# Optimization experiments

Measured on AMD Instinct MI355X. Metric: run time of the kernel, lower is better.

The kernel has to match this reference:

```python
import jax, jax.numpy as jnp
import numpy as np

B, S, T = 64, 256, 32
VS, VT = 4000, 32000
E = H = 512
L = 2
PAD_IDX = 1
BOS_IDX = 2


def setup_inputs() -> dict:
    key = jax.random.key(0)
    ks = jax.random.split(key, 16)
    u = lambda k, sh: jax.random.uniform(k, sh, jnp.float32, -0.08, 0.08)
    inp = {
        'X': jax.random.randint(ks[0], (B, S), 0, VS),
        'y': jax.random.randint(ks[1], (B, T), 0, VT),
        'emb_src': u(ks[2], (VS, E)).at[PAD_IDX].set(0.0),
        'emb_tgt': u(ks[3], (VT, E)).at[PAD_IDX].set(0.0),
        'enc_Wih': u(ks[4], (L, 4 * H, E)),
        'enc_Whh': u(ks[5], (L, 4 * H, H)),
        'enc_bih': u(ks[6], (L, 4 * H)),
        'enc_bhh': u(ks[7], (L, 4 * H)),
        'dec_Wih': u(ks[8], (L, 4 * H, E)),
        'dec_Whh': u(ks[9], (L, 4 * H, H)),
        'dec_bih': u(ks[10], (L, 4 * H)),
        'dec_bhh': u(ks[11], (L, 4 * H)),
        'fcW': u(ks[12], (VT, H)),
        'fcb': u(ks[13], (VT,)),
    }
    return inp


def _cell(x, h, c, Wih, Whh, bih, bhh):
    # PyTorch LSTM cell, gate order i,f,g,o. x:[B,E], h,c:[B,H]
    gates = x @ Wih.T + h @ Whh.T + bih + bhh  # [B,4H]
    i, f, g, o = jnp.split(gates, 4, axis=-1)
    c = jax.nn.sigmoid(f) * c + jax.nn.sigmoid(i) * jnp.tanh(g)
    h = jax.nn.sigmoid(o) * jnp.tanh(c)
    return h, c


def _stack_step(x, hs, cs, Wih, Whh, bih, bhh):
    # run num_layers stacked cells for one timestep; hs,cs: [L,B,H]
    new_h, new_c = [], []
    inp = x
    for l in range(Wih.shape[0]):
        h, c = _cell(inp, hs[l], cs[l], Wih[l], Whh[l], bih[l], bhh[l])
        new_h.append(h)
        new_c.append(c)
        inp = h
    return jnp.stack(new_h), jnp.stack(new_c), inp


def _forward(X, y, emb_src, emb_tgt, enc_Wih, enc_Whh, enc_bih, enc_bhh,
             dec_Wih, dec_Whh, dec_bih, dec_bhh, fcW, fcb):
    b = X.shape[0]
    # ----- encoder: LSTM over full (un-padded) source sequence -----
    xs = emb_src[X].transpose(1, 0, 2)  # [S,B,E] time-major
    h0 = jnp.zeros((L, b, H), xs.dtype)
    c0 = jnp.zeros((L, b, H), xs.dtype)

    def enc_step(carry, x):
        hs, cs = carry
        hs, cs, _ = _stack_step(x, hs, cs, enc_Wih, enc_Whh, enc_bih, enc_bhh)
        return (hs, cs), None

    (hs, cs), _ = jax.lax.scan(enc_step, (h0, c0), xs)

    bos = jnp.full((b, 1), BOS_IDX, y.dtype)
    dec_in = jnp.concatenate([bos, y[:, :-1]], axis=1)  # [B,T]
    toks = dec_in.transpose(1, 0)  # [T,B]

    def dec_step(carry, tok):
        hs, cs = carry
        x = emb_tgt[tok]  # [B,E]
        hs, cs, top = _stack_step(x, hs, cs, dec_Wih, dec_Whh, dec_bih, dec_bhh)
        return (hs, cs), top

    (_, _), tops = jax.lax.scan(dec_step, (hs, cs), toks)  # tops: [T,B,H]
    # model returns only the last time step's log-softmax prediction
    logits = tops[-1] @ fcW.T + fcb  # [B,VT]
    return jax.nn.log_softmax(logits, axis=-1)


def reference(X, y, emb_src, emb_tgt, enc_Wih, enc_Whh, enc_bih, enc_bhh,
              dec_Wih, dec_Whh, dec_bih, dec_bhh, fcW, fcb):
    return _forward(X, y, emb_src, emb_tgt, enc_Wih, enc_Whh, enc_bih, enc_bhh,
                    dec_Wih, dec_Whh, dec_bih, dec_bhh, fcW, fcb)
```

## Files before the change

kernel.cpp:

```cpp
#include <hip/hip_runtime.h>

#define NB 256
#define NT 256

typedef __attribute__((ext_vector_type(8))) short short8;
typedef __attribute__((ext_vector_type(4))) float f32x4;

constexpr int Bz = 64, Sz = 256, Tz = 32, Ez = 512, Hz = 512, G4 = 2048, VT = 32000;

__device__ __forceinline__ unsigned short f2b(float f) {
    unsigned u; __builtin_memcpy(&u, &f, 4);
    u = (u + 0x7fffu + ((u >> 16) & 1u)) >> 16;
    return (unsigned short)u;
}
__device__ __forceinline__ float sgm(float x) { return 1.0f / (1.0f + __expf(-x)); }
__device__ __forceinline__ float tnh(float x) { return 1.0f - 2.0f / (1.0f + __expf(2.0f * x)); }

__global__ __launch_bounds__(NT) void init_kernel(
    unsigned* __restrict__ hbuf_u32, float* __restrict__ row_sums,
    unsigned* __restrict__ bars)
{
    const int idx = blockIdx.x * NT + threadIdx.x;
#pragma unroll
    for (int i = 0; i < 4; ++i) hbuf_u32[idx * 4 + i] = 0u;
    if (blockIdx.x == 0) {
        bars[threadIdx.x] = 0u;
        if (threadIdx.x < 64) row_sums[threadIdx.x] = 0.0f;
    }
}

__global__ __launch_bounds__(NT, 2) void scan_kernel(
    const int* __restrict__ X, const int* __restrict__ Y,
    const float* __restrict__ emb_src, const float* __restrict__ emb_tgt,
    const float* __restrict__ eWih, const float* __restrict__ eWhh,
    const float* __restrict__ ebih, const float* __restrict__ ebhh,
    const float* __restrict__ dWih, const float* __restrict__ dWhh,
    const float* __restrict__ dbih, const float* __restrict__ dbhh,
    unsigned short* __restrict__ hbuf,
    unsigned* __restrict__ bars)
{
    __shared__ __align__(16) unsigned char smem[38144];
    unsigned short* xh_lds = (unsigned short*)smem;
    float* gates_lds = (float*)(smem + 33024);
    float* c_lds     = (float*)(smem + 33024 + 4096);

    const int tid  = threadIdx.x;
    const int bid  = blockIdx.x;
    const int lay  = bid >> 7;
    const int bt   = (bid >> 5) & 3;
    const int ht   = bid & 31;
    const int wave = tid >> 6;
    const int lane = tid & 63;
    const int nl   = lane & 15;
    const int quad = lane >> 4;
    const int srow = tid >> 4;
    const int ssub = tid & 15;
    const int bglob = bt * 16 + srow;

    unsigned* bar_arrive = bars + bt * 64;
    unsigned* bar_flag   = bars + bt * 64 + 32;
    unsigned gen = 0;

    auto barrier = [&]() {
        ++gen;
        __syncthreads();
        if (tid == 0) {
            unsigned old = __hip_atomic_fetch_add(bar_arrive, 1u,
                               __ATOMIC_RELAXED, __HIP_MEMORY_SCOPE_AGENT);
            if (old == gen * 64u - 1u) {
                __hip_atomic_store(bar_flag, gen,
                                   __ATOMIC_RELAXED, __HIP_MEMORY_SCOPE_AGENT);
            } else {
                while (__hip_atomic_load(bar_flag,
                           __ATOMIC_RELAXED, __HIP_MEMORY_SCOPE_AGENT) < gen)
                    __builtin_amdgcn_s_sleep(1);
            }
        }
        __syncthreads();
    };

    c_lds[tid] = 0.0f;
    __syncthreads();

    short8 wfrag[32];
    float bias_r = 0.0f;
    const int r = wave * 512 + ht * 16 + nl;

    auto load_w = [&](const float* Wih, const float* Whh,
                      const float* bih, const float* bhh) {
        const float* wi = Wih + (size_t)(lay * G4 + r) * 512;
        const float* wh = Whh + (size_t)(lay * G4 + r) * 512;
#pragma unroll
        for (int kc = 0; kc < 32; ++kc) {
            const int k0 = kc * 32 + quad * 8;
            const float* s = (k0 < 512) ? (wi + k0) : (wh + (k0 - 512));
            short8 v;
#pragma unroll
            for (int j = 0; j < 8; ++j) v[j] = (short)f2b(s[j]);
            wfrag[kc] = v;
        }
        bias_r = bih[lay * G4 + r] + bhh[lay * G4 + r];
    };

    auto step = [&](const float* xrow_f, const unsigned short* xrow_b,
                    const unsigned short* hrow, unsigned short* hout) {
        {
            unsigned short* d = xh_lds + srow * 1032;
            if (xrow_f) {
                short8* dx = (short8*)(d + ssub * 32);
                const float4* xs = (const float4*)xrow_f;
#pragma unroll
                for (int i = 0; i < 4; ++i) {
                    float4 lo = xs[ssub * 8 + 2 * i];
                    float4 hi = xs[ssub * 8 + 2 * i + 1];
                    short8 v;
                    v[0] = (short)f2b(lo.x); v[1] = (short)f2b(lo.y);
                    v[2] = (short)f2b(lo.z); v[3] = (short)f2b(lo.w);
                    v[4] = (short)f2b(hi.x); v[5] = (short)f2b(hi.y);
                    v[6] = (short)f2b(hi.z); v[7] = (short)f2b(hi.w);
                    dx[i] = v;
                }
            } else {
                const unsigned long long* xs = (const unsigned long long*)xrow_b;
                unsigned long long* dx = (unsigned long long*)(d + ssub * 32);
#pragma unroll
                for (int i = 0; i < 8; ++i)
                    dx[i] = __hip_atomic_load(xs + ssub * 8 + i,
                                __ATOMIC_RELAXED, __HIP_MEMORY_SCOPE_AGENT);
            }
            const unsigned long long* hs = (const unsigned long long*)hrow;
            unsigned long long* dh = (unsigned long long*)(d + 512 + ssub * 32);
#pragma unroll
            for (int i = 0; i < 8; ++i)
                dh[i] = __hip_atomic_load(hs + ssub * 8 + i,
                            __ATOMIC_RELAXED, __HIP_MEMORY_SCOPE_AGENT);
        }
        __syncthreads();
        f32x4 acc = {0.f, 0.f, 0.f, 0.f};
        const unsigned short* ar = xh_lds + nl * 1032 + quad * 8;
#pragma unroll
        for (int kc = 0; kc < 32; ++kc) {
            short8 a = *(const short8*)(ar + kc * 32);
            acc = __builtin_amdgcn_mfma_f32_16x16x32_bf16(a, wfrag[kc], acc, 0, 0, 0);
        }
#pragma unroll
        for (int i = 0; i < 4; ++i) {
            float v = acc[i] + bias_r;
            v = (wave == 2) ? tnh(v) : sgm(v);
            gates_lds[wave * 256 + (quad * 4 + i) * 16 + nl] = v;
        }
        __syncthreads();
        if (tid < 128) {
            const int m = tid >> 3, np = tid & 7;
            float hp[2];
#pragma unroll
            for (int j = 0; j < 2; ++j) {
                const int n = 2 * np + j;
                const float iv = gates_lds[      m * 16 + n];
                const float fv = gates_lds[256 + m * 16 + n];
                const float gv = gates_lds[512 + m * 16 + n];
                const float ov = gates_lds[768 + m * 16 + n];
                float c = c_lds[m * 16 + n];
                c = fv * c + iv * gv;
                c_lds[m * 16 + n] = c;
                hp[j] = ov * tnh(c);
            }
            const unsigned pack = (unsigned)f2b(hp[0]) | ((unsigned)f2b(hp[1]) << 16);
            unsigned* dst = (unsigned*)&hout[(bt * 16 + m) * 512 + ht * 16 + 2 * np];
            __hip_atomic_store(dst, pack, __ATOMIC_RELAXED, __HIP_MEMORY_SCOPE_AGENT);
        }
    };

    auto hb = [&](int l, int p) { return hbuf + (size_t)(l * 2 + p) * Bz * Hz; };

    load_w(eWih, eWhh, ebih, ebhh);
    for (int t = 0; t <= Sz; ++t) {
        if (lay == 0) {
            if (t < Sz) {
                const int tok = X[bglob * Sz + t];
                step(emb_src + (size_t)tok * Ez, nullptr,
                     hb(0, (t + 1) & 1) + bglob * Hz, hb(0, t & 1));
            }
        } else {
            if (t >= 1) {
                const int s = t - 1;
                step(nullptr, hb(0, s & 1) + bglob * Hz,
                     hb(1, (s + 1) & 1) + bglob * Hz, hb(1, s & 1));
            }
        }
        barrier();
    }

    load_w(dWih, dWhh, dbih, dbhh);
    for (int t = 0; t <= Tz; ++t) {
        if (lay == 0) {
            if (t < Tz) {
                const int tok = (t == 0) ? 2 : Y[bglob * Tz + t - 1];
                step(emb_tgt + (size_t)tok * Ez, nullptr,
                     hb(0, (t + 1) & 1) + bglob * Hz, hb(0, t & 1));
            }
        } else {
            if (t >= 1) {
                const int s = t - 1;
                step(nullptr, hb(0, s & 1) + bglob * Hz,
                     hb(1, (s + 1) & 1) + bglob * Hz, hb(1, s & 1));
            }
        }
        barrier();
    }
}

__global__ __launch_bounds__(NT, 1) void fc_kernel(
    const float* __restrict__ fcW, const float* __restrict__ fcb,
    const unsigned short* __restrict__ hbuf,
    float* __restrict__ logits, float* __restrict__ row_sums)
{
    __shared__ __align__(16) unsigned char smem[66816];
    unsigned short* h_lds = (unsigned short*)smem;
    float* row_part = (float*)(smem + 64 * 520 * 2);

    const int tid  = threadIdx.x;
    const int bid  = blockIdx.x;
    const int wave = tid >> 6;
    const int lane = tid & 63;
    const int nl   = lane & 15;
    const int quad = lane >> 4;

    {
        const unsigned short* htop = hbuf + (size_t)3 * Bz * Hz;
        const int rr2 = tid >> 2, pp = tid & 3;
        const short8* s = (const short8*)(htop + rr2 * 512 + pp * 128);
        short8* d = (short8*)(h_lds + rr2 * 520 + pp * 128);
#pragma unroll
        for (int i = 0; i < 16; ++i) d[i] = s[i];
    }
    if (tid < 64) row_part[tid] = 0.f;
    __syncthreads();

    const int c0 = bid * 128;
    f32x4 acc[8];
#pragma unroll
    for (int ct = 0; ct < 8; ++ct) acc[ct] = (f32x4){0.f, 0.f, 0.f, 0.f};
    const unsigned short* ar = h_lds + (wave * 16 + nl) * 520 + quad * 8;
    const float* bb = fcW + ((size_t)c0 + nl) * 512 + quad * 8;
    for (int kc = 0; kc < 16; ++kc) {
        short8 a = *(const short8*)(ar + kc * 32);
#pragma unroll
        for (int ct = 0; ct < 8; ++ct) {
            const float* bp = bb + (size_t)ct * 16 * 512 + kc * 32;
            float4 lo = *(const float4*)(bp);
            float4 hi = *(const float4*)(bp + 4);
            short8 b;
            b[0] = (short)f2b(lo.x); b[1] = (short)f2b(lo.y);
            b[2] = (short)f2b(lo.z); b[3] = (short)f2b(lo.w);
            b[4] = (short)f2b(hi.x); b[5] = (short)f2b(hi.y);
            b[6] = (short)f2b(hi.z); b[7] = (short)f2b(hi.w);
            acc[ct] = __builtin_amdgcn_mfma_f32_16x16x32_bf16(a, b, acc[ct], 0, 0, 0);
        }
    }
    float ls[4] = {0.f, 0.f, 0.f, 0.f};
#pragma unroll
    for (int ct = 0; ct < 8; ++ct) {
        const int col = c0 + ct * 16 + nl;
        const float bias = fcb[col];
#pragma unroll
        for (int i = 0; i < 4; ++i) {
            const float lg = acc[ct][i] + bias;
            logits[(size_t)(wave * 16 + quad * 4 + i) * VT + col] = lg;
            ls[i] += __expf(lg);
        }
    }
#pragma unroll
    for (int i = 0; i < 4; ++i)
        atomicAdd(&row_part[wave * 16 + quad * 4 + i], ls[i]);
    __syncthreads();
    if (tid < 64) atomicAdd(&row_sums[tid], row_part[tid]);
}

__global__ __launch_bounds__(NT) void norm_kernel(
    const float* __restrict__ logits, const float* __restrict__ row_sums,
    float* __restrict__ out)
{
    const int idx = blockIdx.x * NT + threadIdx.x;
    const int row = idx / VT;
    out[idx] = logits[idx] - __logf(row_sums[row]);
}

extern "C" void kernel_launch(void* const* d_in, const int* in_sizes, int n_in,
                              void* d_out, int out_size, void* d_ws, size_t ws_size,
                              hipStream_t stream) {
    const int* X = (const int*)d_in[0];
    const int* Y = (const int*)d_in[1];
    const float* emb_src = (const float*)d_in[2];
    const float* emb_tgt = (const float*)d_in[3];
    const float* eWih = (const float*)d_in[4];
    const float* eWhh = (const float*)d_in[5];
    const float* ebih = (const float*)d_in[6];
    const float* ebhh = (const float*)d_in[7];
    const float* dWih = (const float*)d_in[8];
    const float* dWhh = (const float*)d_in[9];
    const float* dbih = (const float*)d_in[10];
    const float* dbhh = (const float*)d_in[11];
    const float* fcW = (const float*)d_in[12];
    const float* fcb = (const float*)d_in[13];
    float* out = (float*)d_out;

    unsigned short* hbuf = (unsigned short*)d_ws;
    float* row_sums = (float*)((char*)d_ws + 262144);
    unsigned* bars  = (unsigned*)((char*)d_ws + 266240);
    float* logits   = (float*)((char*)d_ws + 524288);

    init_kernel<<<dim3(64), dim3(NT), 0, stream>>>((unsigned*)hbuf, row_sums, bars);

    void* args[] = {&X, &Y, &emb_src, &emb_tgt, &eWih, &eWhh, &ebih, &ebhh,
                    &dWih, &dWhh, &dbih, &dbhh, &hbuf, &bars};
    hipLaunchCooperativeKernel(reinterpret_cast<void*>(scan_kernel),
                               dim3(NB), dim3(NT), args, 0, stream);

    fc_kernel<<<dim3(VT / 128), dim3(NT), 0, stream>>>(fcW, fcb, hbuf, logits, row_sums);

    norm_kernel<<<dim3((Bz * VT) / NT), dim3(NT), 0, stream>>>(logits, row_sums, out);
}
```

Baseline: 1.696 ms.

## Replace counter grid barrier with per-block flag slots and swizzle LDS staging

The single atomic-counter barrier is replaced by per-block generation slots that one wavefront polls together with a wave-wide all-check, which removes the serialized fetch-add contention among 64 blocks every timestep. Row staging now has each wave load whole rows with coalesced 16-byte chunks into an XOR-swizzled LDS layout without padding, and the gate scratch is padded to reduce bank conflicts. The MFMA chain is split into four independent accumulators to shorten the dependency chain. The risks are extra polling traffic from 64 lanes per block and the correctness of the swizzle indexing.

```diff
diff --git a/kernel.cpp b/kernel.cpp
--- a/kernel.cpp
+++ b/kernel.cpp
@@ -5,6 +5,7 @@
 
 typedef __attribute__((ext_vector_type(8))) short short8;
 typedef __attribute__((ext_vector_type(4))) float f32x4;
+typedef __attribute__((ext_vector_type(2))) unsigned long long ull2;
 
 constexpr int Bz = 64, Sz = 256, Tz = 32, Ez = 512, Hz = 512, G4 = 2048, VT = 32000;
 
@@ -39,10 +40,10 @@
     unsigned short* __restrict__ hbuf,
     unsigned* __restrict__ bars)
 {
-    __shared__ __align__(16) unsigned char smem[38144];
+    __shared__ __align__(16) unsigned char smem[39168];
     unsigned short* xh_lds = (unsigned short*)smem;
-    float* gates_lds = (float*)(smem + 33024);
-    float* c_lds     = (float*)(smem + 33024 + 4096);
+    float* gates_lds = (float*)(smem + 32768);
+    float* c_lds     = (float*)(smem + 37888);
 
     const int tid  = threadIdx.x;
     const int bid  = blockIdx.x;
@@ -53,33 +54,29 @@
     const int lane = tid & 63;
     const int nl   = lane & 15;
     const int quad = lane >> 4;
-    const int srow = tid >> 4;
-    const int ssub = tid & 15;
-    const int bglob = bt * 16 + srow;
-
-    unsigned* bar_arrive = bars + bt * 64;
-    unsigned* bar_flag   = bars + bt * 64 + 32;
+
+    unsigned* slots = bars + bt * 64;
+    const int myslot = lay * 32 + ht;
     unsigned gen = 0;
 
     auto barrier = [&]() {
         ++gen;
         __syncthreads();
-        if (tid == 0) {
-            unsigned old = __hip_atomic_fetch_add(bar_arrive, 1u,
-                               __ATOMIC_RELAXED, __HIP_MEMORY_SCOPE_AGENT);
-            if (old == gen * 64u - 1u) {
-                __hip_atomic_store(bar_flag, gen,
+        if (tid < 64) {
+            if (tid == 0)
+                __hip_atomic_store(slots + myslot, gen,
                                    __ATOMIC_RELAXED, __HIP_MEMORY_SCOPE_AGENT);
-            } else {
-                while (__hip_atomic_load(bar_flag,
-                           __ATOMIC_RELAXED, __HIP_MEMORY_SCOPE_AGENT) < gen)
-                    __builtin_amdgcn_s_sleep(1);
+            for (;;) {
+                unsigned v = __hip_atomic_load(slots + tid,
+                                 __ATOMIC_RELAXED, __HIP_MEMORY_SCOPE_AGENT);
+                if (__all((int)(v >= gen))) break;
+                __builtin_amdgcn_s_sleep(1);
             }
         }
         __syncthreads();
     };
 
-    c_lds[tid] = 0.0f;
+    for (int i = tid; i < 320; i += NT) c_lds[i] = 0.0f;
     __syncthreads();
 
     short8 wfrag[32];
@@ -102,52 +99,72 @@
         bias_r = bih[lay * G4 + r] + bhh[lay * G4 + r];
     };
 
-    auto step = [&](const float* xrow_f, const unsigned short* xrow_b,
+    const int kx = (nl >> 2) & 1;
+    const int qx = quad ^ (nl & 3);
+
+    auto step = [&](const float* xtab, const int* tk, const unsigned short* xb,
                     const unsigned short* hrow, unsigned short* hout) {
-        {
-            unsigned short* d = xh_lds + srow * 1032;
-            if (xrow_f) {
-                short8* dx = (short8*)(d + ssub * 32);
-                const float4* xs = (const float4*)xrow_f;
-#pragma unroll
-                for (int i = 0; i < 4; ++i) {
-                    float4 lo = xs[ssub * 8 + 2 * i];
-                    float4 hi = xs[ssub * 8 + 2 * i + 1];
-                    short8 v;
-                    v[0] = (short)f2b(lo.x); v[1] = (short)f2b(lo.y);
-                    v[2] = (short)f2b(lo.z); v[3] = (short)f2b(lo.w);
-                    v[4] = (short)f2b(hi.x); v[5] = (short)f2b(hi.y);
-                    v[6] = (short)f2b(hi.z); v[7] = (short)f2b(hi.w);
-                    dx[i] = v;
-                }
-            } else {
-                const unsigned long long* xs = (const unsigned long long*)xrow_b;
-                unsigned long long* dx = (unsigned long long*)(d + ssub * 32);
-#pragma unroll
-                for (int i = 0; i < 8; ++i)
-                    dx[i] = __hip_atomic_load(xs + ssub * 8 + i,
-                                __ATOMIC_RELAXED, __HIP_MEMORY_SCOPE_AGENT);
-            }
-            const unsigned long long* hs = (const unsigned long long*)hrow;
-            unsigned long long* dh = (unsigned long long*)(d + 512 + ssub * 32);
-#pragma unroll
-            for (int i = 0; i < 8; ++i)
-                dh[i] = __hip_atomic_load(hs + ssub * 8 + i,
-                            __ATOMIC_RELAXED, __HIP_MEMORY_SCOPE_AGENT);
+        const int rb = wave << 2;
+        if (xtab) {
+#pragma unroll
+            for (int rr = 0; rr < 4; ++rr) {
+                const int rw = rb + rr;
+                const float* s = xtab + (size_t)tk[rr] * Ez + (lane << 3);
+                float4 lo = *(const float4*)s;
+                float4 hi = *(const float4*)(s + 4);
+                short8 v;
+                v[0] = (short)f2b(lo.x); v[1] = (short)f2b(lo.y);
+                v[2] = (short)f2b(lo.z); v[3] = (short)f2b(lo.w);
+                v[4] = (short)f2b(hi.x); v[5] = (short)f2b(hi.y);
+                v[6] = (short)f2b(hi.z); v[7] = (short)f2b(hi.w);
+                *(short8*)(xh_lds + (rw << 10) + ((lane ^ (rw & 7)) << 3)) = v;
+            }
+        } else {
+#pragma unroll
+            for (int rr = 0; rr < 4; ++rr) {
+                const int rw = rb + rr;
+                const unsigned long long* s =
+                    (const unsigned long long*)(xb + ((size_t)(bt * 16 + rw) << 9)) + (lane << 1);
+                unsigned long long a = __hip_atomic_load(s,
+                        __ATOMIC_RELAXED, __HIP_MEMORY_SCOPE_AGENT);
+                unsigned long long b = __hip_atomic_load(s + 1,
+                        __ATOMIC_RELAXED, __HIP_MEMORY_SCOPE_AGENT);
+                *(ull2*)(xh_lds + (rw << 10) + ((lane ^ (rw & 7)) << 3)) = (ull2){a, b};
+            }
+        }
+#pragma unroll
+        for (int rr = 0; rr < 4; ++rr) {
+            const int rw = rb + rr;
+            const unsigned long long* s =
+                (const unsigned long long*)(hrow + ((size_t)(bt * 16 + rw) << 9)) + (lane << 1);
+            unsigned long long a = __hip_atomic_load(s,
+                    __ATOMIC_RELAXED, __HIP_MEMORY_SCOPE_AGENT);
+            unsigned long long b = __hip_atomic_load(s + 1,
+                    __ATOMIC_RELAXED, __HIP_MEMORY_SCOPE_AGENT);
+            *(ull2*)(xh_lds + (rw << 10) + 512 + ((lane ^ (rw & 7)) << 3)) = (ull2){a, b};
         }
         __syncthreads();
-        f32x4 acc = {0.f, 0.f, 0.f, 0.f};
-        const unsigned short* ar = xh_lds + nl * 1032 + quad * 8;
-#pragma unroll
-        for (int kc = 0; kc < 32; ++kc) {
-            short8 a = *(const short8*)(ar + kc * 32);
-            acc = __builtin_amdgcn_mfma_f32_16x16x32_bf16(a, wfrag[kc], acc, 0, 0, 0);
-        }
+
+        const unsigned short* arE = xh_lds + (nl << 10) + (qx << 3) + (kx << 5);
+        const unsigned short* arO = xh_lds + (nl << 10) + (qx << 3) - (kx << 5);
+        f32x4 a0 = {0.f, 0.f, 0.f, 0.f}, a1 = a0, a2 = a0, a3 = a0;
+#pragma unroll
+        for (int kc = 0; kc < 32; kc += 4) {
+            short8 x0 = *(const short8*)(arE + ((kc + 0) << 5));
+            short8 x1 = *(const short8*)(arO + ((kc + 1) << 5));
+            short8 x2 = *(const short8*)(arE + ((kc + 2) << 5));
+            short8 x3 = *(const short8*)(arO + ((kc + 3) << 5));
+            a0 = __builtin_amdgcn_mfma_f32_16x16x32_bf16(x0, wfrag[kc + 0], a0, 0, 0, 0);
+            a1 = __builtin_amdgcn_mfma_f32_16x16x32_bf16(x1, wfrag[kc + 1], a1, 0, 0, 0);
+            a2 = __builtin_amdgcn_mfma_f32_16x16x32_bf16(x2, wfrag[kc + 2], a2, 0, 0, 0);
+            a3 = __builtin_amdgcn_mfma_f32_16x16x32_bf16(x3, wfrag[kc + 3], a3, 0, 0, 0);
+        }
+        f32x4 acc = (a0 + a1) + (a2 + a3);
 #pragma unroll
         for (int i = 0; i < 4; ++i) {
             float v = acc[i] + bias_r;
             v = (wave == 2) ? tnh(v) : sgm(v);
-            gates_lds[wave * 256 + (quad * 4 + i) * 16 + nl] = v;
+            gates_lds[wave * 320 + (quad * 4 + i) * 20 + nl] = v;
         }
         __syncthreads();
         if (tid < 128) {
@@ -156,17 +173,17 @@
 #pragma unroll
             for (int j = 0; j < 2; ++j) {
                 const int n = 2 * np + j;
-                const float iv = gates_lds[      m * 16 + n];
-                const float fv = gates_lds[256 + m * 16 + n];
-                const float gv = gates_lds[512 + m * 16 + n];
-                const float ov = gates_lds[768 + m * 16 + n];
-                float c = c_lds[m * 16 + n];
+                const float iv = gates_lds[      m * 20 + n];
+                const float fv = gates_lds[320 + m * 20 + n];
+                const float gv = gates_lds[640 + m * 20 + n];
+                const float ov = gates_lds[960 + m * 20 + n];
+                float c = c_lds[m * 20 + n];
                 c = fv * c + iv * gv;
-                c_lds[m * 16 + n] = c;
+                c_lds[m * 20 + n] = c;
                 hp[j] = ov * tnh(c);
             }
             const unsigned pack = (unsigned)f2b(hp[0]) | ((unsigned)f2b(hp[1]) << 16);
-            unsigned* dst = (unsigned*)&hout[(bt * 16 + m) * 512 + ht * 16 + 2 * np];
+            unsigned* dst = (unsigned*)&hout[(size_t)(bt * 16 + m) * 512 + ht * 16 + 2 * np];
             __hip_atomic_store(dst, pack, __ATOMIC_RELAXED, __HIP_MEMORY_SCOPE_AGENT);
         }
     };
@@ -177,15 +194,17 @@
     for (int t = 0; t <= Sz; ++t) {
         if (lay == 0) {
             if (t < Sz) {
-                const int tok = X[bglob * Sz + t];
-                step(emb_src + (size_t)tok * Ez, nullptr,
-                     hb(0, (t + 1) & 1) + bglob * Hz, hb(0, t & 1));
+                int tk[4];
+#pragma unroll
+                for (int rr = 0; rr < 4; ++rr)
+                    tk[rr] = X[(bt * 16 + (wave << 2) + rr) * Sz + t];
+                step(emb_src, tk, nullptr, hb(0, (t + 1) & 1), hb(0, t & 1));
             }
         } else {
             if (t >= 1) {
                 const int s = t - 1;
-                step(nullptr, hb(0, s & 1) + bglob * Hz,
-                     hb(1, (s + 1) & 1) + bglob * Hz, hb(1, s & 1));
+                step(nullptr, nullptr, hb(0, s & 1),
+                     hb(1, (s + 1) & 1), hb(1, s & 1));
             }
         }
         barrier();
@@ -195,15 +214,17 @@
     for (int t = 0; t <= Tz; ++t) {
         if (lay == 0) {
             if (t < Tz) {
-                const int tok = (t == 0) ? 2 : Y[bglob * Tz + t - 1];
-                step(emb_tgt + (size_t)tok * Ez, nullptr,
-                     hb(0, (t + 1) & 1) + bglob * Hz, hb(0, t & 1));
+                int tk[4];
+#pragma unroll
+                for (int rr = 0; rr < 4; ++rr)
+                    tk[rr] = (t == 0) ? 2 : Y[(bt * 16 + (wave << 2) + rr) * Tz + t - 1];
+                step(emb_tgt, tk, nullptr, hb(0, (t + 1) & 1), hb(0, t & 1));
             }
         } else {
             if (t >= 1) {
                 const int s = t - 1;
-                step(nullptr, hb(0, s & 1) + bglob * Hz,
-                     hb(1, (s + 1) & 1) + bglob * Hz, hb(1, s & 1));
+                step(nullptr, nullptr, hb(0, s & 1),
+                     hb(1, (s + 1) & 1), hb(1, s & 1));
             }
         }
         barrier();
```

After: 1.983 ms. 16.9% more time.
